# Kernel optimization log

Measured on AMD Instinct MI355X. Metric: run time of the kernel, lower is better.

Reference implementation:

```python
import jax, jax.numpy as jnp
import numpy as np

N_RAYS = 262144
N_BINS = 64          # bin edges per ray
N_IMPORTANCE = 128   # fine samples per ray


def setup_inputs() -> dict:
    key = jax.random.key(0)
    k1, k2, k3 = jax.random.split(key, 3)
    # bins must be sorted along last axis (bin edges): cumsum of positive steps
    steps = jax.random.uniform(k1, (N_RAYS, N_BINS), dtype=jnp.float32) + 0.01
    bins = jnp.cumsum(steps, axis=-1)
    weights = jax.random.uniform(k2, (N_RAYS, N_BINS - 1), dtype=jnp.float32)
    # u plays the role of torch.rand t_vals (deterministic=False path)
    u = jax.random.uniform(k3, (N_RAYS, N_IMPORTANCE), dtype=jnp.float32)
    return {"bins": bins, "weights": weights, "u": u, "n_importance": N_IMPORTANCE}


def reference(bins, weights, u, n_importance):
    # weights: [N, M-1]; bins: [N, M]; u: [N, n_importance]
    weights = weights + 1e-5
    pdf = weights / jnp.sum(weights, axis=-1, keepdims=True)
    cdf = jnp.cumsum(pdf, axis=-1)
    cdf = jnp.concatenate([jnp.zeros_like(cdf[..., :1]), cdf], axis=-1)  # [N, M]

    # batched binary search (torch.searchsorted, right=False -> side='left')
    idx = jax.vmap(lambda c, t: jnp.searchsorted(c, t, side='left'))(
        jax.lax.stop_gradient(cdf), u)                                   # [N, I]
    lower = jnp.maximum(idx - 1, 0)
    upper = jnp.minimum(idx, cdf.shape[-1] - 1)

    cdf_lo = jnp.take_along_axis(cdf, lower, axis=-1)
    cdf_hi = jnp.take_along_axis(cdf, upper, axis=-1)
    bins_lo = jnp.take_along_axis(bins, lower, axis=-1)
    bins_hi = jnp.take_along_axis(bins, upper, axis=-1)

    denom = cdf_hi - cdf_lo
    denom = jnp.where(denom < 1e-5, jnp.ones_like(denom), denom)
    t = (u - cdf_lo) / denom
    samples = bins_lo + t * (bins_hi - bins_lo)                          # [N, I]
    return samples
```

## Files before the change

### kernel.cpp

```cpp
#include <hip/hip_runtime.h>


constexpr int NBINS = 64;
constexpr int NW = NBINS - 1;
constexpr int NIMP = 128;
constexpr int WAVES_PER_BLOCK = 4;
constexpr int RAYS_PER_WAVE = 2;
constexpr int RAYS_PER_BLOCK = WAVES_PER_BLOCK * RAYS_PER_WAVE;

template <int Ctrl, int Rm>
__device__ __forceinline__ float dppterm(float x) {
    return __int_as_float(__builtin_amdgcn_update_dpp(
        0, __float_as_int(x), Ctrl, Rm, 0xF, true));
}

__device__ __forceinline__ float rdlane(float x, int lane) {
    return __int_as_float(__builtin_amdgcn_readlane(__float_as_int(x), lane));
}

__device__ __forceinline__ float bperm_f(float x, int lane_idx) {
    return __int_as_float(
        __builtin_amdgcn_ds_bpermute(lane_idx << 2, __float_as_int(x)));
}

__device__ __forceinline__ float wave_incl_scan(float x) {
    x += dppterm<0x111, 0xF>(x);
    x += dppterm<0x112, 0xF>(x);
    x += dppterm<0x114, 0xF>(x);
    x += dppterm<0x118, 0xF>(x);
    x += dppterm<0x142, 0xA>(x);
    x += dppterm<0x143, 0xC>(x);
    return x;
}

struct Pivots { float c8, c16, c24, c32, c40, c48, c56; };

__device__ __forceinline__ Pivots make_pivots(float cdfv) {
    Pivots p;
    p.c8  = rdlane(cdfv, 8);
    p.c16 = rdlane(cdfv, 16);
    p.c24 = rdlane(cdfv, 24);
    p.c32 = rdlane(cdfv, 32);
    p.c40 = rdlane(cdfv, 40);
    p.c48 = rdlane(cdfv, 48);
    p.c56 = rdlane(cdfv, 56);
    return p;
}

__device__ __forceinline__ float sample_one(float uv, const float* cdf,
                                            float cdfv, float bv,
                                            const Pivots& P)
{
    const int grp = (int)(P.c8 < uv) + (int)(P.c16 < uv) + (int)(P.c24 < uv) +
                    (int)(P.c32 < uv) + (int)(P.c40 < uv) + (int)(P.c48 < uv) +
                    (int)(P.c56 < uv);
    const int pos = grp << 3;

    const float4 g0 = *(const float4*)(cdf + pos);
    const float4 g1 = *(const float4*)(cdf + pos + 4);
    const int cnt = (int)(g0.y < uv) + (int)(g0.z < uv) + (int)(g0.w < uv) +
                    (int)(g1.x < uv) + (int)(g1.y < uv) + (int)(g1.z < uv) +
                    (int)(g1.w < uv);

    const int lower = pos + cnt;
    const int upper = (uv > 0.0f) ? (lower + 1) : 0;

    const float lo  = bperm_f(cdfv, lower);
    const float chi = bperm_f(cdfv, upper);
    const float blo = bperm_f(bv, lower);
    const float bhi = bperm_f(bv, upper);

    float denom = chi - lo;
    denom = (denom < 1e-5f) ? 1.0f : denom;
    const float t = (uv - lo) * __builtin_amdgcn_rcpf(denom);
    return __builtin_fmaf(t, bhi - blo, blo);
}

__global__ __launch_bounds__(256) void sample_pdf_kernel(
    const float* __restrict__ bins,
    const float* __restrict__ weights,
    const float* __restrict__ u,
    float* __restrict__ out,
    int n_rays)
{
    __shared__ alignas(16) float s_cdf[WAVES_PER_BLOCK][RAYS_PER_WAVE][NBINS];

    const int wave = threadIdx.x >> 6;
    const int lane = threadIdx.x & 63;
    const int base = blockIdx.x * RAYS_PER_BLOCK + wave * RAYS_PER_WAVE;
    const uint32_t rA = (uint32_t)min(base,     n_rays - 1);
    const uint32_t rB = (uint32_t)min(base + 1, n_rays - 1);

    const float bvA = bins[rA * NBINS + lane];
    const float bvB = bins[rB * NBINS + lane];
    const float wA = (lane < NW) ? (weights[rA * NW + lane] + 1e-5f) : 0.0f;
    const float wB = (lane < NW) ? (weights[rB * NW + lane] + 1e-5f) : 0.0f;
    const float2 uuA = ((const float2*)u)[rA * (NIMP / 2) + lane];
    const float2 uuB = ((const float2*)u)[rB * (NIMP / 2) + lane];

    const float SA = wave_incl_scan(wA);
    const float SB = wave_incl_scan(wB);
    float cdfvA = (SA - wA) * __builtin_amdgcn_rcpf(rdlane(SA, 63));
    float cdfvB = (SB - wB) * __builtin_amdgcn_rcpf(rdlane(SB, 63));
    if (lane == NBINS - 1) { cdfvA = 1.0f; cdfvB = 1.0f; }

    s_cdf[wave][0][lane] = cdfvA;
    s_cdf[wave][1][lane] = cdfvB;

    const Pivots PA = make_pivots(cdfvA);
    const Pivots PB = make_pivots(cdfvB);

    const float* cA = s_cdf[wave][0];
    const float* cB = s_cdf[wave][1];

    float2 resA, resB;
    resA.x = sample_one(uuA.x, cA, cdfvA, bvA, PA);
    resA.y = sample_one(uuA.y, cA, cdfvA, bvA, PA);
    resB.x = sample_one(uuB.x, cB, cdfvB, bvB, PB);
    resB.y = sample_one(uuB.y, cB, cdfvB, bvB, PB);

    ((float2*)out)[rA * (NIMP / 2) + lane] = resA;
    ((float2*)out)[rB * (NIMP / 2) + lane] = resB;
}

extern "C" void kernel_launch(void* const* d_in, const int* in_sizes, int n_in,
                              void* d_out, int out_size, void* d_ws, size_t ws_size,
                              hipStream_t stream) {
    const float* bins    = (const float*)d_in[0];
    const float* weights = (const float*)d_in[1];
    const float* u       = (const float*)d_in[2];
    float* out = (float*)d_out;

    const int n_rays = in_sizes[0] / NBINS;
    const int grid = (n_rays + RAYS_PER_BLOCK - 1) / RAYS_PER_BLOCK;
    sample_pdf_kernel<<<grid, 256, 0, stream>>>(bins, weights, u, out, n_rays);
}
```

Baseline: 304.0 us.

## Use persistent grid-stride waves with software-prefetched next ray pair

Replaces the one-block-per-eight-rays launch with a grid capped at 2048 blocks in which each wave loops over ray pairs. Global loads for the next pair are issued before computing the current pair, so memory latency overlaps with the scan and search work. This cuts block launch overhead and hides load latency, but it raises register pressure and reduces the number of waves in flight, which could lower occupancy-based latency hiding on a memory-bound kernel.

```diff
diff --git a/kernel.cpp b/kernel.cpp
--- a/kernel.cpp
+++ b/kernel.cpp
@@ -5,8 +5,7 @@
 constexpr int NW = NBINS - 1;
 constexpr int NIMP = 128;
 constexpr int WAVES_PER_BLOCK = 4;
-constexpr int RAYS_PER_WAVE = 2;
-constexpr int RAYS_PER_BLOCK = WAVES_PER_BLOCK * RAYS_PER_WAVE;
+constexpr int MAX_BLOCKS = 2048;
 
 template <int Ctrl, int Rm>
 __device__ __forceinline__ float dppterm(float x) {
@@ -76,6 +75,20 @@
     return __builtin_fmaf(t, bhi - blo, blo);
 }
 
+struct RayBuf { float bv, w; float2 uu; };
+
+__device__ __forceinline__ RayBuf issue_loads(
+    const float* __restrict__ bins, const float* __restrict__ weights,
+    const float* __restrict__ u, uint32_t r, int lane)
+{
+    RayBuf b;
+    b.bv = bins[r * NBINS + lane];
+    b.w = 0.0f;
+    if (lane < NW) b.w = weights[r * NW + lane];
+    b.uu = ((const float2*)u)[r * (NIMP / 2) + lane];
+    return b;
+}
+
 __global__ __launch_bounds__(256) void sample_pdf_kernel(
     const float* __restrict__ bins,
     const float* __restrict__ weights,
@@ -83,44 +96,64 @@
     float* __restrict__ out,
     int n_rays)
 {
-    __shared__ alignas(16) float s_cdf[WAVES_PER_BLOCK][RAYS_PER_WAVE][NBINS];
+    __shared__ alignas(16) float s_cdf[WAVES_PER_BLOCK][2][NBINS];
 
     const int wave = threadIdx.x >> 6;
     const int lane = threadIdx.x & 63;
-    const int base = blockIdx.x * RAYS_PER_BLOCK + wave * RAYS_PER_WAVE;
-    const uint32_t rA = (uint32_t)min(base,     n_rays - 1);
-    const uint32_t rB = (uint32_t)min(base + 1, n_rays - 1);
+    const int gwave  = blockIdx.x * WAVES_PER_BLOCK + wave;
+    const int nwaves = gridDim.x * WAVES_PER_BLOCK;
+    const int npairs = (n_rays + 1) >> 1;
 
-    const float bvA = bins[rA * NBINS + lane];
-    const float bvB = bins[rB * NBINS + lane];
-    const float wA = (lane < NW) ? (weights[rA * NW + lane] + 1e-5f) : 0.0f;
-    const float wB = (lane < NW) ? (weights[rB * NW + lane] + 1e-5f) : 0.0f;
-    const float2 uuA = ((const float2*)u)[rA * (NIMP / 2) + lane];
-    const float2 uuB = ((const float2*)u)[rB * (NIMP / 2) + lane];
+    float* cA = s_cdf[wave][0];
+    float* cB = s_cdf[wave][1];
 
-    const float SA = wave_incl_scan(wA);
-    const float SB = wave_incl_scan(wB);
-    float cdfvA = (SA - wA) * __builtin_amdgcn_rcpf(rdlane(SA, 63));
-    float cdfvB = (SB - wB) * __builtin_amdgcn_rcpf(rdlane(SB, 63));
-    if (lane == NBINS - 1) { cdfvA = 1.0f; cdfvB = 1.0f; }
+    int p = gwave;
+    {
+        const int pc = min(p, npairs - 1);
+        const uint32_t rA = (uint32_t)min(2 * pc,     n_rays - 1);
+        const uint32_t rB = (uint32_t)min(2 * pc + 1, n_rays - 1);
+        RayBuf a0 = issue_loads(bins, weights, u, rA, lane);
+        RayBuf a1 = issue_loads(bins, weights, u, rB, lane);
 
-    s_cdf[wave][0][lane] = cdfvA;
-    s_cdf[wave][1][lane] = cdfvB;
+        while (p < npairs) {
+            const int pn = p + nwaves;
+            const int pc2 = min(pn, npairs - 1);
+            const uint32_t rA2 = (uint32_t)min(2 * pc2,     n_rays - 1);
+            const uint32_t rB2 = (uint32_t)min(2 * pc2 + 1, n_rays - 1);
+            RayBuf b0 = issue_loads(bins, weights, u, rA2, lane);
+            RayBuf b1 = issue_loads(bins, weights, u, rB2, lane);
 
-    const Pivots PA = make_pivots(cdfvA);
-    const Pivots PB = make_pivots(cdfvB);
+            const uint32_t r0 = (uint32_t)min(2 * p,     n_rays - 1);
+            const uint32_t r1 = (uint32_t)min(2 * p + 1, n_rays - 1);
 
-    const float* cA = s_cdf[wave][0];
-    const float* cB = s_cdf[wave][1];
+            const float wA = (lane < NW) ? (a0.w + 1e-5f) : 0.0f;
+            const float wB = (lane < NW) ? (a1.w + 1e-5f) : 0.0f;
+            const float SA = wave_incl_scan(wA);
+            const float SB = wave_incl_scan(wB);
+            float cdfvA = (SA - wA) * __builtin_amdgcn_rcpf(rdlane(SA, 63));
+            float cdfvB = (SB - wB) * __builtin_amdgcn_rcpf(rdlane(SB, 63));
+            if (lane == NBINS - 1) { cdfvA = 1.0f; cdfvB = 1.0f; }
 
-    float2 resA, resB;
-    resA.x = sample_one(uuA.x, cA, cdfvA, bvA, PA);
-    resA.y = sample_one(uuA.y, cA, cdfvA, bvA, PA);
-    resB.x = sample_one(uuB.x, cB, cdfvB, bvB, PB);
-    resB.y = sample_one(uuB.y, cB, cdfvB, bvB, PB);
+            cA[lane] = cdfvA;
+            cB[lane] = cdfvB;
 
-    ((float2*)out)[rA * (NIMP / 2) + lane] = resA;
-    ((float2*)out)[rB * (NIMP / 2) + lane] = resB;
+            const Pivots PA = make_pivots(cdfvA);
+            const Pivots PB = make_pivots(cdfvB);
+
+            float2 resA, resB;
+            resA.x = sample_one(a0.uu.x, cA, cdfvA, a0.bv, PA);
+            resA.y = sample_one(a0.uu.y, cA, cdfvA, a0.bv, PA);
+            resB.x = sample_one(a1.uu.x, cB, cdfvB, a1.bv, PB);
+            resB.y = sample_one(a1.uu.y, cB, cdfvB, a1.bv, PB);
+
+            ((float2*)out)[r0 * (NIMP / 2) + lane] = resA;
+            ((float2*)out)[r1 * (NIMP / 2) + lane] = resB;
+
+            a0 = b0;
+            a1 = b1;
+            p = pn;
+        }
+    }
 }
 
 extern "C" void kernel_launch(void* const* d_in, const int* in_sizes, int n_in,
@@ -132,6 +165,8 @@
     float* out = (float*)d_out;
 
     const int n_rays = in_sizes[0] / NBINS;
-    const int grid = (n_rays + RAYS_PER_BLOCK - 1) / RAYS_PER_BLOCK;
-    sample_pdf_kernel<<<grid, 256, 0, stream>>>(bins, weights, u, out, n_rays);
+    const int npairs = (n_rays + 1) / 2;
+    int blocks = (npairs + WAVES_PER_BLOCK - 1) / WAVES_PER_BLOCK;
+    if (blocks > MAX_BLOCKS) blocks = MAX_BLOCKS;
+    sample_pdf_kernel<<<blocks, 256, 0, stream>>>(bins, weights, u, out, n_rays);
 }
```

Measured after the change: 322.4 us. 6.0% more time.

## Stage cdf and bins rows in LDS, select via compare-mux, four rays per wave

Applied to the files above, without the earlier changes.

Stores both cdf and bin values per ray in shared memory and picks the bracketing pair with a predicated select chain over the loaded 8-element window, replacing the four ds_bpermute lookups. Doubles rays per wave to 4 and issues all global loads up front, with an asm barrier forcing them before compute, to expose more memory-level parallelism. The trade is more LDS reads and VGPR use per ray, which may lower occupancy.

```diff
diff --git a/kernel.cpp b/kernel.cpp
--- a/kernel.cpp
+++ b/kernel.cpp
@@ -5,8 +5,9 @@
 constexpr int NW = NBINS - 1;
 constexpr int NIMP = 128;
 constexpr int WAVES_PER_BLOCK = 4;
-constexpr int RAYS_PER_WAVE = 2;
+constexpr int RAYS_PER_WAVE = 4;
 constexpr int RAYS_PER_BLOCK = WAVES_PER_BLOCK * RAYS_PER_WAVE;
+constexpr int ROW = 2 * NBINS;
 
 template <int Ctrl, int Rm>
 __device__ __forceinline__ float dppterm(float x) {
@@ -16,11 +17,6 @@
 
 __device__ __forceinline__ float rdlane(float x, int lane) {
     return __int_as_float(__builtin_amdgcn_readlane(__float_as_int(x), lane));
-}
-
-__device__ __forceinline__ float bperm_f(float x, int lane_idx) {
-    return __int_as_float(
-        __builtin_amdgcn_ds_bpermute(lane_idx << 2, __float_as_int(x)));
 }
 
 __device__ __forceinline__ float wave_incl_scan(float x) {
@@ -47,8 +43,7 @@
     return p;
 }
 
-__device__ __forceinline__ float sample_one(float uv, const float* cdf,
-                                            float cdfv, float bv,
+__device__ __forceinline__ float sample_mux(float uv, const float* row,
                                             const Pivots& P)
 {
     const int grp = (int)(P.c8 < uv) + (int)(P.c16 < uv) + (int)(P.c24 < uv) +
@@ -56,19 +51,23 @@
                     (int)(P.c56 < uv);
     const int pos = grp << 3;
 
-    const float4 g0 = *(const float4*)(cdf + pos);
-    const float4 g1 = *(const float4*)(cdf + pos + 4);
-    const int cnt = (int)(g0.y < uv) + (int)(g0.z < uv) + (int)(g0.w < uv) +
-                    (int)(g1.x < uv) + (int)(g1.y < uv) + (int)(g1.z < uv) +
-                    (int)(g1.w < uv);
+    const float4 w0 = *(const float4*)(row + pos);
+    const float4 w1 = *(const float4*)(row + pos + 4);
+    const float4 b0 = *(const float4*)(row + NBINS + pos);
+    const float4 b1 = *(const float4*)(row + NBINS + pos + 4);
+    const float w8 = row[pos + 8];
+    const float b8 = row[NBINS + pos + 8];
 
-    const int lower = pos + cnt;
-    const int upper = (uv > 0.0f) ? (lower + 1) : 0;
-
-    const float lo  = bperm_f(cdfv, lower);
-    const float chi = bperm_f(cdfv, upper);
-    const float blo = bperm_f(bv, lower);
-    const float bhi = bperm_f(bv, upper);
+    const bool c1 = w0.y < uv, c2 = w0.z < uv, c3 = w0.w < uv, c4 = w1.x < uv,
+               c5 = w1.y < uv, c6 = w1.z < uv, c7 = w1.w < uv;
+    float lo = w0.x, chi = w0.y, blo = b0.x, bhi = b0.y;
+    if (c1) { lo = w0.y; chi = w0.z; blo = b0.y; bhi = b0.z; }
+    if (c2) { lo = w0.z; chi = w0.w; blo = b0.z; bhi = b0.w; }
+    if (c3) { lo = w0.w; chi = w1.x; blo = b0.w; bhi = b1.x; }
+    if (c4) { lo = w1.x; chi = w1.y; blo = b1.x; bhi = b1.y; }
+    if (c5) { lo = w1.y; chi = w1.z; blo = b1.y; bhi = b1.z; }
+    if (c6) { lo = w1.z; chi = w1.w; blo = b1.z; bhi = b1.w; }
+    if (c7) { lo = w1.w; chi = w8;   blo = b1.w; bhi = b8;   }
 
     float denom = chi - lo;
     denom = (denom < 1e-5f) ? 1.0f : denom;
@@ -83,44 +82,56 @@
     float* __restrict__ out,
     int n_rays)
 {
-    __shared__ alignas(16) float s_cdf[WAVES_PER_BLOCK][RAYS_PER_WAVE][NBINS];
+    __shared__ alignas(16) float s[WAVES_PER_BLOCK * RAYS_PER_WAVE * ROW + 8];
 
     const int wave = threadIdx.x >> 6;
     const int lane = threadIdx.x & 63;
     const int base = blockIdx.x * RAYS_PER_BLOCK + wave * RAYS_PER_WAVE;
-    const uint32_t rA = (uint32_t)min(base,     n_rays - 1);
-    const uint32_t rB = (uint32_t)min(base + 1, n_rays - 1);
 
-    const float bvA = bins[rA * NBINS + lane];
-    const float bvB = bins[rB * NBINS + lane];
-    const float wA = (lane < NW) ? (weights[rA * NW + lane] + 1e-5f) : 0.0f;
-    const float wB = (lane < NW) ? (weights[rB * NW + lane] + 1e-5f) : 0.0f;
-    const float2 uuA = ((const float2*)u)[rA * (NIMP / 2) + lane];
-    const float2 uuB = ((const float2*)u)[rB * (NIMP / 2) + lane];
+    uint32_t r[RAYS_PER_WAVE];
+    #pragma unroll
+    for (int i = 0; i < RAYS_PER_WAVE; ++i)
+        r[i] = (uint32_t)min(base + i, n_rays - 1);
 
-    const float SA = wave_incl_scan(wA);
-    const float SB = wave_incl_scan(wB);
-    float cdfvA = (SA - wA) * __builtin_amdgcn_rcpf(rdlane(SA, 63));
-    float cdfvB = (SB - wB) * __builtin_amdgcn_rcpf(rdlane(SB, 63));
-    if (lane == NBINS - 1) { cdfvA = 1.0f; cdfvB = 1.0f; }
+    float bv[RAYS_PER_WAVE], wr[RAYS_PER_WAVE];
+    float2 uu[RAYS_PER_WAVE];
+    #pragma unroll
+    for (int i = 0; i < RAYS_PER_WAVE; ++i) {
+        bv[i] = bins[r[i] * NBINS + lane];
+        wr[i] = 0.0f;
+        if (lane < NW) wr[i] = weights[r[i] * NW + lane];
+        uu[i] = ((const float2*)u)[r[i] * (NIMP / 2) + lane];
+    }
+    asm volatile("" :: "v"(bv[0]), "v"(bv[1]), "v"(bv[2]), "v"(bv[3]),
+                       "v"(wr[0]), "v"(wr[1]), "v"(wr[2]), "v"(wr[3]),
+                       "v"(uu[0].x), "v"(uu[0].y), "v"(uu[1].x), "v"(uu[1].y),
+                       "v"(uu[2].x), "v"(uu[2].y), "v"(uu[3].x), "v"(uu[3].y));
 
-    s_cdf[wave][0][lane] = cdfvA;
-    s_cdf[wave][1][lane] = cdfvB;
+    float cdfv[RAYS_PER_WAVE];
+    #pragma unroll
+    for (int i = 0; i < RAYS_PER_WAVE; ++i) {
+        const float w = (lane < NW) ? (wr[i] + 1e-5f) : 0.0f;
+        const float S = wave_incl_scan(w);
+        float c = (S - w) * __builtin_amdgcn_rcpf(rdlane(S, 63));
+        if (lane == NBINS - 1) c = 1.0f;
+        cdfv[i] = c;
+        float* row = s + (wave * RAYS_PER_WAVE + i) * ROW;
+        row[lane] = c;
+        row[NBINS + lane] = bv[i];
+    }
 
-    const Pivots PA = make_pivots(cdfvA);
-    const Pivots PB = make_pivots(cdfvB);
+    Pivots P[RAYS_PER_WAVE];
+    #pragma unroll
+    for (int i = 0; i < RAYS_PER_WAVE; ++i) P[i] = make_pivots(cdfv[i]);
 
-    const float* cA = s_cdf[wave][0];
-    const float* cB = s_cdf[wave][1];
-
-    float2 resA, resB;
-    resA.x = sample_one(uuA.x, cA, cdfvA, bvA, PA);
-    resA.y = sample_one(uuA.y, cA, cdfvA, bvA, PA);
-    resB.x = sample_one(uuB.x, cB, cdfvB, bvB, PB);
-    resB.y = sample_one(uuB.y, cB, cdfvB, bvB, PB);
-
-    ((float2*)out)[rA * (NIMP / 2) + lane] = resA;
-    ((float2*)out)[rB * (NIMP / 2) + lane] = resB;
+    #pragma unroll
+    for (int i = 0; i < RAYS_PER_WAVE; ++i) {
+        const float* row = s + (wave * RAYS_PER_WAVE + i) * ROW;
+        float2 res;
+        res.x = sample_mux(uu[i].x, row, P[i]);
+        res.y = sample_mux(uu[i].y, row, P[i]);
+        ((float2*)out)[r[i] * (NIMP / 2) + lane] = res;
+    }
 }
 
 extern "C" void kernel_launch(void* const* d_in, const int* in_sizes, int n_in,
```

After: 329.7 us. 8.4% more time.
